# Optimization experiments

Measured on AMD Instinct MI355X. Metric: run time of the kernel, lower is better.

## Reference

```python
import jax, jax.numpy as jnp
import numpy as np

NUM_HEADS = 16
MAX_FREQ = 10.0
LN_EPS = 1e-5
PI = float(np.pi)


def layer_norm(x, w, b):
    mu = jnp.mean(x, axis=-1, keepdims=True)
    var = jnp.mean(jnp.square(x - mu), axis=-1, keepdims=True)
    return (x - mu) * jax.lax.rsqrt(var + LN_EPS) * w + b


def rotate_half(x):
    # interleaved pairs: (x0,x1,x2,x3,...) -> (-x1,x0,-x3,x2,...)
    x1 = x[..., 0::2]
    x2 = x[..., 1::2]
    return jnp.stack((-x2, x1), axis=-1).reshape(x.shape)


def drofe(q, k, freqband, demo):
    # q, k: [B,H,N,D]; freqband: [N,2] (lower/upper band bound); demo: [B,2] (age, gender)
    D = q.shape[-1]
    freqs = jnp.linspace(1.0, MAX_FREQ / 2.0, D // 4).astype(q.dtype) * PI  # [D/4]
    ang = jnp.concatenate([freqband[:, 0:1] * freqs, freqband[:, 1:2] * freqs], axis=-1)  # [N, D/2]
    ang = jnp.repeat(ang, 2, axis=-1)  # [N, D]
    cos, sin = jnp.cos(ang), jnp.sin(ang)
    age = demo[:, 0][:, None, None, None]
    gender = demo[:, 1][:, None, None, None]
    q = q * cos * age + rotate_half(q) * sin * gender
    k = k * cos * age + rotate_half(k) * sin * gender
    return q, k


def setup_inputs() -> dict:
    key = jax.random.key(0)
    ks = jax.random.split(key, 16)
    B, N, C, F = 8, 1024, 1024, 4096
    s = 0.02
    return {
        "x": jax.random.normal(ks[0], (B, N, C), jnp.float32),
        "demographic_info": jax.random.uniform(ks[1], (B, 2), jnp.float32),
        "explanation": jax.random.normal(ks[2], (B, N, C), jnp.float32),
        "freqband": jax.random.uniform(ks[3], (N, 2), jnp.float32) * 50.0,
        "w_qkv": jax.random.normal(ks[4], (C, 3 * C), jnp.float32) * s,
        "w_proj": jax.random.normal(ks[5], (C, C), jnp.float32) * s,
        "b_proj": jnp.zeros((C,), jnp.float32),
        "gamma1": jnp.full((C,), 1e-5, jnp.float32),
        "gamma2": jnp.full((C,), 1e-5, jnp.float32),
        "ln1_w": jnp.ones((C,), jnp.float32),
        "ln1_b": jnp.zeros((C,), jnp.float32),
        "ln2_w": jnp.ones((C,), jnp.float32),
        "ln2_b": jnp.zeros((C,), jnp.float32),
        "w1": jax.random.normal(ks[6], (C, F), jnp.float32) * s,
        "b1": jnp.zeros((F,), jnp.float32),
        "w2": jax.random.normal(ks[7], (F, C), jnp.float32) * s,
        "b2": jnp.zeros((C,), jnp.float32),
    }


def reference(x, demographic_info, explanation, freqband, w_qkv, w_proj, b_proj,
              gamma1, gamma2, ln1_w, ln1_b, ln2_w, ln2_b, w1, b1, w2, b2):
    B, N, C = x.shape
    H = NUM_HEADS
    D = C // H

    def split_qkv(t):
        return (t @ w_qkv).reshape(B, N, 3, H, D).transpose(2, 0, 3, 1, 4)  # [3,B,H,N,D]

    v = split_qkv(x)[2]
    qkv_e = split_qkv(explanation)  # explanation-swap: q,k come from explanation
    q, k = qkv_e[0], qkv_e[1]
    q, k = drofe(q, k, freqband, demographic_info)

    attn = jax.nn.softmax(jnp.einsum('bhnd,bhmd->bhnm', q, k) * (D ** -0.5), axis=-1)
    o = jnp.einsum('bhnm,bhmd->bhnd', attn, v).transpose(0, 2, 1, 3).reshape(B, N, C)
    o = o @ w_proj + b_proj

    x = layer_norm(x + gamma1 * o, ln1_w, ln1_b)  # post-norm + LayerScale
    h = jax.nn.gelu(x @ w1 + b1, approximate=False) @ w2 + b2
    x = layer_norm(x + gamma2 * h, ln2_w, ln2_b)
    return x
```

## Files before the change

kernel.cpp:

```cpp
#include <hip/hip_runtime.h>
#include <hip/hip_bf16.h>
#include <math.h>

typedef __attribute__((ext_vector_type(8))) short bf16x8;
typedef __attribute__((ext_vector_type(8))) unsigned short u16x8;
typedef __attribute__((ext_vector_type(4))) float f32x4;
typedef __attribute__((ext_vector_type(4))) unsigned short u16x4;

__device__ inline unsigned short f2bf(float f) {
    union { float f; unsigned u; } v; v.f = f;
    unsigned r = (v.u + 0x7fff + ((v.u >> 16) & 1)) >> 16;
    return (unsigned short)r;
}
__device__ inline float bf2f(unsigned short u) {
    union { unsigned u; float f; } v; v.u = ((unsigned)u) << 16; return v.f;
}

#define GLL16(gp, lp) __builtin_amdgcn_global_load_lds(                      \
    (const __attribute__((address_space(1))) void*)(gp),                     \
    (__attribute__((address_space(3))) void*)(lp), 16, 0, 0)

#define BAR() do { asm volatile("" ::: "memory");                            \
    __builtin_amdgcn_s_barrier();                                            \
    asm volatile("" ::: "memory"); } while (0)
#define VMW10() asm volatile("s_waitcnt vmcnt(10)" ::: "memory")

template<int EPI>
__global__ __launch_bounds__(512, 2) void gemm8p(
    const unsigned short* __restrict__ A,
    const unsigned short* __restrict__ Bt,
    const float* __restrict__ bias,
    unsigned short* __restrict__ Cout,
    unsigned short* __restrict__ Cout2,
    const float* __restrict__ fbq,
    const float* __restrict__ demo,
    int M, int Nn, int K, int ldc)
{
    __shared__ unsigned char lds[131072];
    const int tid = threadIdx.x;
    const int w = tid >> 6, lane = tid & 63;
    const int lk = lane & 15, lg = lane >> 4;
    const int wr = w >> 2, wc = w & 3;
    const int nbn = Nn >> 8;
    const int nb = gridDim.x;
    int bid = blockIdx.x;
    int swz = (nb & 7) ? bid : (bid & 7) * (nb >> 3) + (bid >> 3);
    const int bm = (swz / nbn) << 8, bn = (swz % nbn) << 8;

    f32x4 acc[8][4] = {};
    bf16x8 af[4][2];
    bf16x8 bfr[2][2][2];

    auto stageH = [&](int buf, int op, int half, int kt) {
        #pragma unroll
        for (int i = 0; i < 2; ++i) {
            int s = tid + i * 512;
            int r = s >> 3, c = s & 7;
            int cs = c ^ (r & 7);
            const unsigned short* gp = (op == 0)
                ? A  + (size_t)(bm + half * 128 + r) * K + kt + cs * 8
                : Bt + (size_t)(bn + half * 128 + r) * K + kt + cs * 8;
            GLL16(gp, &lds[buf * 65536 + op * 32768 + half * 16384 + s * 16]);
        }
    };
    auto rdA = [&](int buf, int ah) {
        #pragma unroll
        for (int ml = 0; ml < 4; ++ml) {
            int row = (ah * 4 + ml) * 32 + wr * 16 + lk;
            #pragma unroll
            for (int kk = 0; kk < 2; ++kk) {
                int sl = (kk * 4 + lg) ^ (row & 7);
                af[ml][kk] = *(const bf16x8*)&lds[buf * 65536 + row * 128 + sl * 16];
            }
        }
    };
    auto rdB = [&](int buf, int g) {
        #pragma unroll
        for (int njl = 0; njl < 2; ++njl) {
            int row = (g * 2 + njl) * 64 + wc * 16 + lk;
            #pragma unroll
            for (int kk = 0; kk < 2; ++kk) {
                int sl = (kk * 4 + lg) ^ (row & 7);
                bfr[g][njl][kk] = *(const bf16x8*)&lds[buf * 65536 + 32768 + row * 128 + sl * 16];
            }
        }
    };
    auto mfmaq = [&](int ah, int g) {
        __builtin_amdgcn_s_setprio(1);
        #pragma unroll
        for (int ml = 0; ml < 4; ++ml)
            #pragma unroll
            for (int njl = 0; njl < 2; ++njl)
                #pragma unroll
                for (int kk = 0; kk < 2; ++kk)
                    acc[ah * 4 + ml][g * 2 + njl] =
                        __builtin_amdgcn_mfma_f32_16x16x32_bf16(
                            af[ml][kk], bfr[g][njl][kk],
                            acc[ah * 4 + ml][g * 2 + njl], 0, 0, 0);
        __builtin_amdgcn_s_setprio(0);
    };

    const int NT = K >> 6;
    stageH(0, 0, 0, 0);
    stageH(0, 1, 0, 0);
    stageH(0, 1, 1, 0);
    stageH(0, 0, 1, 0);
    stageH(1, 0, 0, 64);
    stageH(1, 1, 0, 64);
    stageH(1, 1, 1, 64);
    VMW10(); BAR();

    for (int t = 0; t < NT; ++t) {
        const int buf = t & 1;
        const int t1 = (t + 1 < NT) ? t + 1 : NT - 1;
        const int t2 = (t + 2 < NT) ? t + 2 : NT - 1;
        const int k1 = t1 << 6, k2 = t2 << 6;
        rdA(buf, 0); rdB(buf, 0);
        stageH(buf ^ 1, 0, 1, k1);
        mfmaq(0, 0);
        VMW10(); BAR();
        rdB(buf, 1);
        stageH(buf, 0, 0, k2);
        mfmaq(0, 1);
        VMW10(); BAR();
        rdA(buf, 1);
        stageH(buf, 1, 0, k2);
        mfmaq(1, 0);
        BAR();
        stageH(buf, 1, 1, k2);
        mfmaq(1, 1);
        VMW10(); BAR();
    }
    asm volatile("s_waitcnt vmcnt(0)" ::: "memory");
    BAR();

    if (EPI == 3) {
        const float PI_F = 3.14159265358979323846f;
        const int b_ = bm >> 10;
        const float age = demo[b_ * 2 + 0], gen = demo[b_ * 2 + 1];
        #pragma unroll
        for (int mi = 0; mi < 8; ++mi) {
            #pragma unroll
            for (int nj = 0; nj < 4; ++nj) {
                int col = bn + nj * 64 + wc * 16 + lk;
                int i = (col & 63) >> 1;
                int ii = (i < 16) ? i : i - 16;
                float freq = (1.0f + (float)ii * (4.0f / 15.0f)) * PI_F;
                int fsel = (i >= 16) ? 1 : 0;
                #pragma unroll
                for (int r = 0; r < 4; ++r) {
                    int row = bm + mi * 32 + wr * 16 + lg * 4 + r;
                    float val = acc[mi][nj][r];
                    float par = __shfl_xor(val, 1);
                    int nn = row & 1023;
                    float ang = fbq[nn * 2 + fsel] * freq;
                    float sv, cv;
                    __sincosf(ang, &sv, &cv);
                    float ca = cv * age, sg = sv * gen;
                    float res = (col & 1) ? (val * ca + par * sg)
                                          : (val * ca - par * sg);
                    if (col < 1024)
                        Cout[(size_t)row * 1024 + col] = f2bf(res * 0.125f);
                    else
                        Cout2[(size_t)row * 1024 + col - 1024] = f2bf(res);
                }
            }
        }
        return;
    }

    #pragma unroll
    for (int mi = 0; mi < 8; ++mi) {
        int row = bm + mi * 32 + wr * 16 + lg * 4;
        #pragma unroll
        for (int nj = 0; nj < 4; ++nj) {
            int col = bn + nj * 64 + wc * 16 + lk;
            #pragma unroll
            for (int r = 0; r < 4; ++r) {
                float v = acc[mi][nj][r] + bias[col];
                if (EPI == 2) {
                    float u = v * 0.7978845608f * (1.0f + 0.044715f * v * v);
                    v = v / (1.0f + __expf(-2.0f * u));
                }
                Cout[(size_t)(row + r) * ldc + col] = f2bf(v);
            }
        }
    }
}

template<int EPI, int OUT_BF>
__global__ __launch_bounds__(256, 4) void gemm2ph128(
    const unsigned short* __restrict__ A,
    const unsigned short* __restrict__ Bt,
    const float* __restrict__ bias,
    void* __restrict__ Cout,
    int M, int Nn, int K, int ldc)
{
    __shared__ unsigned char lds[2][16384];
    const int tid = threadIdx.x;
    const int w = tid >> 6, lane = tid & 63;
    const int lk = lane & 15, lg = lane >> 4;
    const int wr = w >> 1, wc = w & 1;
    const int nbn = Nn >> 7;
    const int nb = gridDim.x;
    int bid = blockIdx.x;
    int swz = (nb & 7) ? bid : (bid & 7) * (nb >> 3) + (bid >> 3);
    const int bm = (swz / nbn) << 7, bn = (swz % nbn) << 7;

    f32x4 acc[4][4] = {};

    auto stage = [&](int buf, int k0) {
        #pragma unroll
        for (int i = 0; i < 4; ++i) {
            int s = tid + i * 256;
            int r = s >> 2, c = s & 3;
            int cs = (c ^ r ^ (r >> 2)) & 3;
            const unsigned short* gp = (r < 128)
                ? A  + (size_t)(bm + r) * K + k0 + cs * 8
                : Bt + (size_t)(bn + (r - 128)) * K + k0 + cs * 8;
            GLL16(gp, &lds[buf][s * 16]);
        }
    };

    const int NT = K >> 5;
    stage(0, 0);
    __syncthreads();
    int cur = 0;
    for (int t = 0; t < NT; ++t) {
        if (t + 1 < NT) stage(cur ^ 1, (t + 1) << 5);
        bf16x8 af[4], bfr[4];
        #pragma unroll
        for (int m = 0; m < 4; ++m) {
            int row = wr * 64 + m * 16 + lk;
            int sl = (lg ^ row ^ (row >> 2)) & 3;
            af[m] = *(const bf16x8*)&lds[cur][row * 64 + sl * 16];
        }
        #pragma unroll
        for (int n = 0; n < 4; ++n) {
            int row = wc * 64 + n * 16 + lk;
            int sl = (lg ^ row ^ (row >> 2)) & 3;
            bfr[n] = *(const bf16x8*)&lds[cur][8192 + row * 64 + sl * 16];
        }
        #pragma unroll
        for (int m = 0; m < 4; ++m)
            #pragma unroll
            for (int n = 0; n < 4; ++n)
                acc[m][n] = __builtin_amdgcn_mfma_f32_16x16x32_bf16(af[m], bfr[n], acc[m][n], 0, 0, 0);
        __syncthreads();
        cur ^= 1;
    }

    #pragma unroll
    for (int m = 0; m < 4; ++m) {
        int row = bm + wr * 64 + m * 16 + lg * 4;
        #pragma unroll
        for (int n = 0; n < 4; ++n) {
            int col = bn + wc * 64 + n * 16 + lk;
            #pragma unroll
            for (int r = 0; r < 4; ++r) {
                float v = acc[m][n][r];
                if (EPI >= 1) v += bias[col];
                if (EPI == 2) {
                    float u = v * 0.7978845608f * (1.0f + 0.044715f * v * v);
                    v = v / (1.0f + __expf(-2.0f * u));
                }
                if (OUT_BF)
                    ((unsigned short*)Cout)[(size_t)(row + r) * ldc + col] = f2bf(v);
                else
                    ((float*)Cout)[(size_t)(row + r) * ldc + col] = v;
            }
        }
    }
}

__global__ __launch_bounds__(256) void cvt_bf16(
    const float* __restrict__ src, unsigned short* __restrict__ dst, int n)
{
    int i = (blockIdx.x * 256 + threadIdx.x) * 4;
    if (i < n) {
        float4 v = *(const float4*)(src + i);
        u16x4 o = { f2bf(v.x), f2bf(v.y), f2bf(v.z), f2bf(v.w) };
        *(u16x4*)(dst + i) = o;
    }
}

__global__ __launch_bounds__(256) void transpose_cvt(
    const float* __restrict__ src, unsigned short* __restrict__ dst, int R, int Cc)
{
    __shared__ float t[32][33];
    const int bc = blockIdx.x * 32, br = blockIdx.y * 32;
    const int tx = threadIdx.x & 31, ty = threadIdx.x >> 5;
    #pragma unroll
    for (int i = 0; i < 4; ++i)
        t[ty + i * 8][tx] = src[(size_t)(br + ty + i * 8) * Cc + bc + tx];
    __syncthreads();
    #pragma unroll
    for (int i = 0; i < 4; ++i)
        dst[(size_t)(bc + ty + i * 8) * R + br + tx] = f2bf(t[tx][ty + i * 8]);
}

__global__ __launch_bounds__(256, 4) void attn_mfma(
    const unsigned short* __restrict__ Q, const unsigned short* __restrict__ K,
    const unsigned short* __restrict__ V, unsigned short* __restrict__ O,
    int B, int H, int N)
{
    __shared__ unsigned short Ks[64 * 64];
    __shared__ unsigned short Vt[64 * 72];
    __shared__ unsigned short Ps[4][16 * 72];

    const int bi = blockIdx.x;
    const int bh = (bi & 7) + 8 * ((bi >> 3) & 15);
    const int q0 = (bi >> 7) * 128;
    const int b = bh >> 4, h = bh & 15;
    const int tid = threadIdx.x;
    const int w = tid >> 6, lane = tid & 63;
    const int lg = lane >> 4, lk = lane & 15;

    bf16x8 qf[2][2];
    #pragma unroll
    for (int qt = 0; qt < 2; ++qt) {
        const unsigned short* qrow =
            Q + (size_t)(b * N + q0 + qt * 64 + w * 16 + lk) * 1024 + h * 64;
        qf[qt][0] = *(const bf16x8*)(qrow + lg * 8);
        qf[qt][1] = *(const bf16x8*)(qrow + 32 + lg * 8);
    }

    f32x4 o[2][4] = {};
    float m_run[2] = { -INFINITY, -INFINITY }, l_run[2] = { 0.f, 0.f };

    for (int t0 = 0; t0 < N; t0 += 64) {
        const size_t kvbase = (size_t)(b * N + t0) * 1024 + h * 64;
        #pragma unroll
        for (int it = 0; it < 2; ++it) {
            int s = it * 256 + tid;
            int row = s >> 3, cb = (s & 7) << 4;
            int dby = cb ^ ((row & 7) << 4);
            GLL16(K + kvbase + (size_t)row * 1024 + (dby >> 1), &Ks[s * 8]);
        }
        {
            int c = tid >> 5, k0 = (tid & 31) * 2;
            const unsigned short* vp = V + kvbase + (size_t)k0 * 1024 + c * 8;
            u16x8 va = *(const u16x8*)vp;
            u16x8 vb = *(const u16x8*)(vp + 1024);
            #pragma unroll
            for (int j = 0; j < 8; ++j) {
                unsigned val = (unsigned)va[j] | ((unsigned)vb[j] << 16);
                *(unsigned*)&Vt[(c * 8 + j) * 72 + k0] = val;
            }
        }
        __syncthreads();

        #pragma unroll
        for (int qt = 0; qt < 2; ++qt) {
            f32x4 s4[4];
            __builtin_amdgcn_s_setprio(1);
            #pragma unroll
            for (int sub = 0; sub < 4; ++sub) {
                f32x4 acc = {0.f, 0.f, 0.f, 0.f};
                #pragma unroll
                for (int kh = 0; kh < 2; ++kh) {
                    int cc = (kh * 64 + lg * 16) ^ ((lk & 7) << 4);
                    bf16x8 kf = *(const bf16x8*)&Ks[(sub * 16 + lk) * 64 + (cc >> 1)];
                    acc = __builtin_amdgcn_mfma_f32_16x16x32_bf16(kf, qf[qt][kh], acc, 0, 0, 0);
                }
                s4[sub] = acc;
            }
            __builtin_amdgcn_s_setprio(0);

            float pmax = -INFINITY;
            #pragma unroll
            for (int sub = 0; sub < 4; ++sub)
                #pragma unroll
                for (int r = 0; r < 4; ++r) pmax = fmaxf(pmax, s4[sub][r]);
            pmax = fmaxf(pmax, __shfl_xor(pmax, 16));
            pmax = fmaxf(pmax, __shfl_xor(pmax, 32));

            if (!__all(pmax - m_run[qt] <= 8.0f)) {
                float mn = fmaxf(m_run[qt], pmax);
                float corr = __expf(m_run[qt] - mn);
                m_run[qt] = mn;
                l_run[qt] *= corr;
                #pragma unroll
                for (int ds = 0; ds < 4; ++ds)
                    #pragma unroll
                    for (int r = 0; r < 4; ++r) o[qt][ds][r] *= corr;
            }

            float psum = 0.f;
            unsigned pw[4][2];
            #pragma unroll
            for (int sub = 0; sub < 4; ++sub) {
                float p0 = __expf(s4[sub][0] - m_run[qt]);
                float p1 = __expf(s4[sub][1] - m_run[qt]);
                float p2 = __expf(s4[sub][2] - m_run[qt]);
                float p3 = __expf(s4[sub][3] - m_run[qt]);
                psum += (p0 + p1) + (p2 + p3);
                pw[sub][0] = (__float_as_uint(p0) >> 16) | (__float_as_uint(p1) & 0xffff0000u);
                pw[sub][1] = (__float_as_uint(p2) >> 16) | (__float_as_uint(p3) & 0xffff0000u);
            }
            psum += __shfl_xor(psum, 16);
            psum += __shfl_xor(psum, 32);
            l_run[qt] += psum;
            #pragma unroll
            for (int sub = 0; sub < 4; ++sub) {
                *(unsigned*)&Ps[w][lk * 72 + sub * 16 + lg * 4]     = pw[sub][0];
                *(unsigned*)&Ps[w][lk * 72 + sub * 16 + lg * 4 + 2] = pw[sub][1];
            }
            asm volatile("s_waitcnt lgkmcnt(0)" ::: "memory");

            __builtin_amdgcn_s_setprio(1);
            #pragma unroll
            for (int kh = 0; kh < 2; ++kh) {
                bf16x8 pf = *(const bf16x8*)&Ps[w][lk * 72 + kh * 32 + lg * 8];
                #pragma unroll
                for (int ds = 0; ds < 4; ++ds) {
                    bf16x8 vf = *(const bf16x8*)&Vt[(ds * 16 + lk) * 72 + kh * 32 + lg * 8];
                    o[qt][ds] = __builtin_amdgcn_mfma_f32_16x16x32_bf16(vf, pf, o[qt][ds], 0, 0, 0);
                }
            }
            __builtin_amdgcn_s_setprio(0);
        }
        __syncthreads();
    }

    #pragma unroll
    for (int qt = 0; qt < 2; ++qt) {
        unsigned short* orow =
            O + (size_t)(b * N + q0 + qt * 64 + w * 16 + lk) * 1024 + h * 64;
        float rinv = 1.0f / l_run[qt];
        #pragma unroll
        for (int ds = 0; ds < 4; ++ds) {
            u16x4 pk = { f2bf(o[qt][ds][0] * rinv), f2bf(o[qt][ds][1] * rinv),
                         f2bf(o[qt][ds][2] * rinv), f2bf(o[qt][ds][3] * rinv) };
            *(u16x4*)(orow + ds * 16 + lg * 4) = pk;
        }
    }
}

template<int XBF>
__global__ __launch_bounds__(256) void ln_res3(
    const void* __restrict__ xv, const unsigned short* __restrict__ y1,
    const float* __restrict__ gamma, const float* __restrict__ w,
    const float* __restrict__ bia, float* __restrict__ out,
    unsigned short* __restrict__ out_bf, int C)
{
    const int row = blockIdx.x;
    __shared__ float buf[1024];
    __shared__ float red[8];
    const size_t base = (size_t)row * C;
    float s = 0.f, ss = 0.f;
    for (int c = threadIdx.x; c < C; c += 256) {
        float xf = XBF ? bf2f(((const unsigned short*)xv)[base + c])
                       : ((const float*)xv)[base + c];
        float v = xf + gamma[c] * bf2f(y1[base + c]);
        buf[c] = v; s += v; ss += v * v;
    }
    #pragma unroll
    for (int msk = 1; msk < 64; msk <<= 1) { s += __shfl_xor(s, msk); ss += __shfl_xor(ss, msk); }
    int wv = threadIdx.x >> 6, lane = threadIdx.x & 63;
    if (lane == 0) { red[wv * 2] = s; red[wv * 2 + 1] = ss; }
    __syncthreads();
    if (threadIdx.x == 0) {
        float S = 0.f, SS = 0.f;
        #pragma unroll
        for (int i = 0; i < 4; ++i) { S += red[2 * i]; SS += red[2 * i + 1]; }
        red[0] = S; red[1] = SS;
    }
    __syncthreads();
    float mu = red[0] / C;
    float var = red[1] / C - mu * mu;
    float rstd = rsqrtf(var + 1e-5f);
    for (int c = threadIdx.x; c < C; c += 256) {
        float v = (buf[c] - mu) * rstd * w[c] + bia[c];
        if (out) out[base + c] = v;
        if (out_bf) out_bf[base + c] = f2bf(v);
    }
}

extern "C" void kernel_launch(void* const* d_in, const int* in_sizes, int n_in,
                              void* d_out, int out_size, void* d_ws, size_t ws_size,
                              hipStream_t stream)
{
    const float* x      = (const float*)d_in[0];
    const float* demo   = (const float*)d_in[1];
    const float* expl   = (const float*)d_in[2];
    const float* fb     = (const float*)d_in[3];
    const float* w_qkv  = (const float*)d_in[4];
    const float* w_proj = (const float*)d_in[5];
    const float* b_proj = (const float*)d_in[6];
    const float* gamma1 = (const float*)d_in[7];
    const float* gamma2 = (const float*)d_in[8];
    const float* ln1_w  = (const float*)d_in[9];
    const float* ln1_b  = (const float*)d_in[10];
    const float* ln2_w  = (const float*)d_in[11];
    const float* ln2_b  = (const float*)d_in[12];
    const float* w1     = (const float*)d_in[13];
    const float* b1     = (const float*)d_in[14];
    const float* w2     = (const float*)d_in[15];
    const float* b2     = (const float*)d_in[16];
    float* out = (float*)d_out;

    const int B = 8, N = 1024, C = 1024, F = 4096, H = 16;
    const int M = B * N;
    const size_t Mi = 1048576;

    float* ws = (float*)d_ws;
    unsigned short* Obf  = (unsigned short*)ws;
    unsigned short* H2   = (unsigned short*)ws;
    unsigned short* Qbf  = (unsigned short*)(ws + 8 * Mi);
    unsigned short* Kbf  = (unsigned short*)(ws + 12 * Mi);
    unsigned short* Vbf  = (unsigned short*)(ws + 16 * Mi);
    unsigned short* Hid  = (unsigned short*)(ws + 8 * Mi);
    unsigned short* Ebf  = (unsigned short*)(ws + 24 * Mi);
    unsigned short* Xbf  = (unsigned short*)(ws + 28 * Mi);
    unsigned short* Pb   = (unsigned short*)(ws + 24 * Mi);
    unsigned short* X1bf = (unsigned short*)(ws + 40 * Mi);
    unsigned short* Wt   = (unsigned short*)(ws + 44 * Mi);
    unsigned short* wqkvT  = Wt;
    unsigned short* wprojT = Wt + (size_t)3145728;
    unsigned short* w1T    = wprojT + (size_t)1048576;
    unsigned short* w2T    = w1T + (size_t)4194304;

    dim3 blk(256);
    dim3 blk5(512);
    const int MC = M * C;

    hipLaunchKernelGGL(cvt_bf16, dim3(MC / 1024), blk, 0, stream, expl, Ebf, MC);
    hipLaunchKernelGGL(cvt_bf16, dim3(MC / 1024), blk, 0, stream, x, Xbf, MC);
    hipLaunchKernelGGL(transpose_cvt, dim3(96, 32), blk, 0, stream, w_qkv, wqkvT, C, 3 * C);
    hipLaunchKernelGGL(transpose_cvt, dim3(32, 32), blk, 0, stream, w_proj, wprojT, C, C);
    hipLaunchKernelGGL(transpose_cvt, dim3(128, 32), blk, 0, stream, w1, w1T, C, F);
    hipLaunchKernelGGL(transpose_cvt, dim3(32, 128), blk, 0, stream, w2, w2T, F, C);

    hipLaunchKernelGGL((gemm8p<3>), dim3(32 * 8), blk5, 0, stream, Ebf, wqkvT,
                       (const float*)nullptr, Qbf, Kbf, fb, demo, M, 2048, C, 2048);
    hipLaunchKernelGGL((gemm2ph128<0,1>), dim3(64 * 8), blk, 0, stream, Xbf,
                       wqkvT + (size_t)2048 * 1024, (const float*)nullptr, (void*)Vbf,
                       M, 1024, C, 1024);

    hipLaunchKernelGGL(attn_mfma, dim3(B * H * (N / 128)), blk, 0, stream, Qbf, Kbf, Vbf, Obf, B, H, N);

    hipLaunchKernelGGL((gemm2ph128<1,1>), dim3(64 * 8), blk, 0, stream, Obf, wprojT, b_proj,
                       (void*)Pb, M, 1024, C, 1024);

    hipLaunchKernelGGL((ln_res3<0>), dim3(M), blk, 0, stream, (const void*)x, Pb,
                       gamma1, ln1_w, ln1_b, (float*)nullptr, X1bf, C);

    hipLaunchKernelGGL((gemm8p<2>), dim3(32 * 16), blk5, 0, stream, X1bf, w1T, b1,
                       Hid, (unsigned short*)nullptr, (const float*)nullptr, (const float*)nullptr,
                       M, F, C, F);
    hipLaunchKernelGGL((gemm2ph128<1,1>), dim3(64 * 8), blk, 0, stream, Hid, w2T, b2,
                       (void*)H2, M, 1024, F, 1024);

    hipLaunchKernelGGL((ln_res3<1>), dim3(M), blk, 0, stream, (const void*)X1bf, H2,
                       gamma2, ln2_w, ln2_b, out, (unsigned short*)nullptr, C);
}
```

Measured before the change: 386.5 us.

## Replace 128x128 two-phase GEMM with 8-wave 128x256 pipelined GEMM for N=1024 projections

Adds gemm8pB, a 512-thread, 128x256-tile GEMM with BK=64. It uses staged global-to-LDS loads, triple-depth prefetch across double buffers, XOR-swizzled LDS and interleaved MFMA quarters with setprio. It replaces the simple 128x128 double-buffered kernel for the V projection, output projection and FFN down projection. The aim is better latency hiding and more data reuse per block. The cost is fewer blocks (256) on a large GPU, 96KB of LDS per block, and fine-grained vmcnt tuning that must match the load counts.

```diff
diff --git a/kernel.cpp b/kernel.cpp
--- a/kernel.cpp
+++ b/kernel.cpp
@@ -23,7 +23,7 @@
 #define BAR() do { asm volatile("" ::: "memory");                            \
     __builtin_amdgcn_s_barrier();                                            \
     asm volatile("" ::: "memory"); } while (0)
-#define VMW10() asm volatile("s_waitcnt vmcnt(10)" ::: "memory")
+#define VMW(n) asm volatile("s_waitcnt vmcnt(" #n ")" ::: "memory")
 
 template<int EPI>
 __global__ __launch_bounds__(512, 2) void gemm8p(
@@ -108,7 +108,7 @@
     stageH(1, 0, 0, 64);
     stageH(1, 1, 0, 64);
     stageH(1, 1, 1, 64);
-    VMW10(); BAR();
+    VMW(10); BAR();
 
     for (int t = 0; t < NT; ++t) {
         const int buf = t & 1;
@@ -118,20 +118,20 @@
         rdA(buf, 0); rdB(buf, 0);
         stageH(buf ^ 1, 0, 1, k1);
         mfmaq(0, 0);
-        VMW10(); BAR();
+        VMW(10); BAR();
         rdB(buf, 1);
         stageH(buf, 0, 0, k2);
         mfmaq(0, 1);
-        VMW10(); BAR();
+        VMW(10); BAR();
         rdA(buf, 1);
         stageH(buf, 1, 0, k2);
         mfmaq(1, 0);
         BAR();
         stageH(buf, 1, 1, k2);
         mfmaq(1, 1);
-        VMW10(); BAR();
-    }
-    asm volatile("s_waitcnt vmcnt(0)" ::: "memory");
+        VMW(10); BAR();
+    }
+    VMW(0);
     BAR();
 
     if (EPI == 3) {
@@ -188,86 +188,128 @@
     }
 }
 
-template<int EPI, int OUT_BF>
-__global__ __launch_bounds__(256, 4) void gemm2ph128(
+template<int EPI>
+__global__ __launch_bounds__(512, 2) void gemm8pB(
     const unsigned short* __restrict__ A,
     const unsigned short* __restrict__ Bt,
     const float* __restrict__ bias,
-    void* __restrict__ Cout,
+    unsigned short* __restrict__ Cout,
     int M, int Nn, int K, int ldc)
 {
-    __shared__ unsigned char lds[2][16384];
+    __shared__ unsigned char lds[98304];
     const int tid = threadIdx.x;
     const int w = tid >> 6, lane = tid & 63;
     const int lk = lane & 15, lg = lane >> 4;
-    const int wr = w >> 1, wc = w & 1;
-    const int nbn = Nn >> 7;
+    const int wr = w >> 2, wc = w & 3;
+    const int nbn = Nn >> 8;
     const int nb = gridDim.x;
     int bid = blockIdx.x;
     int swz = (nb & 7) ? bid : (bid & 7) * (nb >> 3) + (bid >> 3);
-    const int bm = (swz / nbn) << 7, bn = (swz % nbn) << 7;
+    const int bm = (swz / nbn) << 7, bn = (swz % nbn) << 8;
 
     f32x4 acc[4][4] = {};
-
-    auto stage = [&](int buf, int k0) {
-        #pragma unroll
-        for (int i = 0; i < 4; ++i) {
-            int s = tid + i * 256;
-            int r = s >> 2, c = s & 3;
-            int cs = (c ^ r ^ (r >> 2)) & 3;
-            const unsigned short* gp = (r < 128)
-                ? A  + (size_t)(bm + r) * K + k0 + cs * 8
-                : Bt + (size_t)(bn + (r - 128)) * K + k0 + cs * 8;
-            GLL16(gp, &lds[buf][s * 16]);
-        }
-    };
-
-    const int NT = K >> 5;
-    stage(0, 0);
-    __syncthreads();
-    int cur = 0;
+    bf16x8 af[2][2];
+    bf16x8 bfr[2][2][2];
+
+    auto stageA = [&](int buf, int half, int kt) {
+        int s = tid;
+        int r = s >> 3, c = s & 7;
+        int cs = c ^ (r & 7);
+        GLL16(A + (size_t)(bm + half * 64 + r) * K + kt + cs * 8,
+              &lds[buf * 49152 + half * 8192 + s * 16]);
+    };
+    auto stageB = [&](int buf, int half, int kt) {
+        #pragma unroll
+        for (int i = 0; i < 2; ++i) {
+            int s = tid + i * 512;
+            int r = s >> 3, c = s & 7;
+            int cs = c ^ (r & 7);
+            GLL16(Bt + (size_t)(bn + half * 128 + r) * K + kt + cs * 8,
+                  &lds[buf * 49152 + 16384 + half * 16384 + s * 16]);
+        }
+    };
+    auto rdA = [&](int buf, int ah) {
+        #pragma unroll
+        for (int ml = 0; ml < 2; ++ml) {
+            int row = (ah * 2 + ml) * 32 + wr * 16 + lk;
+            #pragma unroll
+            for (int kk = 0; kk < 2; ++kk) {
+                int sl = (kk * 4 + lg) ^ (row & 7);
+                af[ml][kk] = *(const bf16x8*)&lds[buf * 49152 + row * 128 + sl * 16];
+            }
+        }
+    };
+    auto rdB = [&](int buf, int g) {
+        #pragma unroll
+        for (int njl = 0; njl < 2; ++njl) {
+            int row = (g * 2 + njl) * 64 + wc * 16 + lk;
+            #pragma unroll
+            for (int kk = 0; kk < 2; ++kk) {
+                int sl = (kk * 4 + lg) ^ (row & 7);
+                bfr[g][njl][kk] = *(const bf16x8*)&lds[buf * 49152 + 16384 + row * 128 + sl * 16];
+            }
+        }
+    };
+    auto mfmaq = [&](int ah, int g) {
+        __builtin_amdgcn_s_setprio(1);
+        #pragma unroll
+        for (int ml = 0; ml < 2; ++ml)
+            #pragma unroll
+            for (int njl = 0; njl < 2; ++njl)
+                #pragma unroll
+                for (int kk = 0; kk < 2; ++kk)
+                    acc[ah * 2 + ml][g * 2 + njl] =
+                        __builtin_amdgcn_mfma_f32_16x16x32_bf16(
+                            af[ml][kk], bfr[g][njl][kk],
+                            acc[ah * 2 + ml][g * 2 + njl], 0, 0, 0);
+        __builtin_amdgcn_s_setprio(0);
+    };
+
+    const int NT = K >> 6;
+    stageA(0, 0, 0);
+    stageB(0, 0, 0);
+    stageB(0, 1, 0);
+    stageA(0, 1, 0);
+    stageA(1, 0, 64);
+    stageB(1, 0, 64);
+    stageB(1, 1, 64);
+    VMW(8); BAR();
+
     for (int t = 0; t < NT; ++t) {
-        if (t + 1 < NT) stage(cur ^ 1, (t + 1) << 5);
-        bf16x8 af[4], bfr[4];
-        #pragma unroll
-        for (int m = 0; m < 4; ++m) {
-            int row = wr * 64 + m * 16 + lk;
-            int sl = (lg ^ row ^ (row >> 2)) & 3;
-            af[m] = *(const bf16x8*)&lds[cur][row * 64 + sl * 16];
-        }
-        #pragma unroll
-        for (int n = 0; n < 4; ++n) {
-            int row = wc * 64 + n * 16 + lk;
-            int sl = (lg ^ row ^ (row >> 2)) & 3;
-            bfr[n] = *(const bf16x8*)&lds[cur][8192 + row * 64 + sl * 16];
-        }
-        #pragma unroll
-        for (int m = 0; m < 4; ++m)
-            #pragma unroll
-            for (int n = 0; n < 4; ++n)
-                acc[m][n] = __builtin_amdgcn_mfma_f32_16x16x32_bf16(af[m], bfr[n], acc[m][n], 0, 0, 0);
-        __syncthreads();
-        cur ^= 1;
-    }
-
-    #pragma unroll
-    for (int m = 0; m < 4; ++m) {
-        int row = bm + wr * 64 + m * 16 + lg * 4;
-        #pragma unroll
-        for (int n = 0; n < 4; ++n) {
-            int col = bn + wc * 64 + n * 16 + lk;
+        const int buf = t & 1;
+        const int t1 = (t + 1 < NT) ? t + 1 : NT - 1;
+        const int t2 = (t + 2 < NT) ? t + 2 : NT - 1;
+        const int k1 = t1 << 6, k2 = t2 << 6;
+        rdA(buf, 0); rdB(buf, 0);
+        stageA(buf ^ 1, 1, k1);
+        mfmaq(0, 0);
+        VMW(7); BAR();
+        rdB(buf, 1);
+        stageA(buf, 0, k2);
+        mfmaq(0, 1);
+        VMW(7); BAR();
+        rdA(buf, 1);
+        stageB(buf, 0, k2);
+        mfmaq(1, 0);
+        BAR();
+        stageB(buf, 1, k2);
+        mfmaq(1, 1);
+        VMW(8); BAR();
+    }
+    VMW(0);
+    BAR();
+
+    #pragma unroll
+    for (int mi = 0; mi < 4; ++mi) {
+        int row = bm + mi * 32 + wr * 16 + lg * 4;
+        #pragma unroll
+        for (int nj = 0; nj < 4; ++nj) {
+            int col = bn + nj * 64 + wc * 16 + lk;
             #pragma unroll
             for (int r = 0; r < 4; ++r) {
-                float v = acc[m][n][r];
+                float v = acc[mi][nj][r];
                 if (EPI >= 1) v += bias[col];
-                if (EPI == 2) {
-                    float u = v * 0.7978845608f * (1.0f + 0.044715f * v * v);
-                    v = v / (1.0f + __expf(-2.0f * u));
-                }
-                if (OUT_BF)
-                    ((unsigned short*)Cout)[(size_t)(row + r) * ldc + col] = f2bf(v);
-                else
-                    ((float*)Cout)[(size_t)(row + r) * ldc + col] = v;
+                Cout[(size_t)(row + r) * ldc + col] = f2bf(v);
             }
         }
     }
@@ -534,14 +576,14 @@
 
     hipLaunchKernelGGL((gemm8p<3>), dim3(32 * 8), blk5, 0, stream, Ebf, wqkvT,
                        (const float*)nullptr, Qbf, Kbf, fb, demo, M, 2048, C, 2048);
-    hipLaunchKernelGGL((gemm2ph128<0,1>), dim3(64 * 8), blk, 0, stream, Xbf,
-                       wqkvT + (size_t)2048 * 1024, (const float*)nullptr, (void*)Vbf,
+    hipLaunchKernelGGL((gemm8pB<0>), dim3(64 * 4), blk5, 0, stream, Xbf,
+                       wqkvT + (size_t)2048 * 1024, (const float*)nullptr, Vbf,
                        M, 1024, C, 1024);
 
     hipLaunchKernelGGL(attn_mfma, dim3(B * H * (N / 128)), blk, 0, stream, Qbf, Kbf, Vbf, Obf, B, H, N);
 
-    hipLaunchKernelGGL((gemm2ph128<1,1>), dim3(64 * 8), blk, 0, stream, Obf, wprojT, b_proj,
-                       (void*)Pb, M, 1024, C, 1024);
+    hipLaunchKernelGGL((gemm8pB<1>), dim3(64 * 4), blk5, 0, stream, Obf, wprojT, b_proj,
+                       Pb, M, 1024, C, 1024);
 
     hipLaunchKernelGGL((ln_res3<0>), dim3(M), blk, 0, stream, (const void*)x, Pb,
                        gamma1, ln1_w, ln1_b, (float*)nullptr, X1bf, C);
@@ -549,8 +591,8 @@
     hipLaunchKernelGGL((gemm8p<2>), dim3(32 * 16), blk5, 0, stream, X1bf, w1T, b1,
                        Hid, (unsigned short*)nullptr, (const float*)nullptr, (const float*)nullptr,
                        M, F, C, F);
-    hipLaunchKernelGGL((gemm2ph128<1,1>), dim3(64 * 8), blk, 0, stream, Hid, w2T, b2,
-                       (void*)H2, M, 1024, F, 1024);
+    hipLaunchKernelGGL((gemm8pB<1>), dim3(64 * 4), blk5, 0, stream, Hid, w2T, b2,
+                       H2, M, 1024, F, 1024);
 
     hipLaunchKernelGGL((ln_res3<1>), dim3(M), blk, 0, stream, (const void*)X1bf, H2,
                        gamma2, ln2_w, ln2_b, out, (unsigned short*)nullptr, C);
```

Result: no change. 388.3 us (+0.5%).
